# Performance work log

Measured on AMD Instinct MI355X. Metric: run time of the kernel, lower is better.

The kernel has to match this reference:

```python
import jax, jax.numpy as jnp
import numpy as np

NUM_GENES = 4384
D_MODEL = 128


def setup_inputs() -> dict:
    key = jax.random.key(0)
    ks = jax.random.split(key, 8)
    B = 8
    return {
        "mutation_input": jax.random.normal(ks[0], (B, NUM_GENES, 4), dtype=jnp.float32),
        "external_V": jax.random.normal(ks[1], (NUM_GENES, D_MODEL), dtype=jnp.float32),
        "W_in": jax.random.normal(ks[2], (4, D_MODEL), dtype=jnp.float32) * 0.5,
        "b_in": jnp.zeros((D_MODEL,), dtype=jnp.float32),
        "key_param": jax.random.normal(ks[3], (NUM_GENES, D_MODEL), dtype=jnp.float32),
        "W1": jax.random.normal(ks[4], (D_MODEL, 64), dtype=jnp.float32) * (1.0 / np.sqrt(D_MODEL)),
        "b1": jnp.zeros((64,), dtype=jnp.float32),
        "W2": jax.random.normal(ks[5], (64, 26), dtype=jnp.float32) * 0.125,
        "b2": jnp.zeros((26,), dtype=jnp.float32),
    }


def reference(mutation_input, external_V, W_in, b_in, key_param, W1, b1, W2, b2):
    # Q: [B, G, D]
    Q = jnp.einsum("bgf,fd->bgd", mutation_input, W_in) + b_in
    scale = 1.0 / jnp.sqrt(jnp.asarray(Q.shape[-1], Q.dtype))
    # scores: [B, G, G] -- full matrix as in the original module
    scores = jnp.einsum("bqd,kd->bqk", Q, key_param) * scale
    attn = jax.nn.softmax(scores, axis=-1)
    # attention output: [B, G, D]
    attn_out = jnp.einsum("bqk,kd->bqd", attn, external_V)
    mean_out = attn_out.mean(axis=1)  # [B, D]
    h = jax.nn.gelu(mean_out @ W1 + b1, approximate=False)
    out = h @ W2 + b2  # [B, 26]
    return out
```

## Files before the change

### kernel.cpp

```cpp
#include <hip/hip_runtime.h>
#include <hip/hip_bf16.h>

#define NUM_GENES 4384
#define GPAD 4608
#define DM 128
#define ROWB 256
#define LDS_STRIDE 272
#define NTILES 137
#define RB_BLOCKS 18
#define NCHUNK 6
#define TPC 23

typedef __attribute__((ext_vector_type(8))) short short8;
typedef __attribute__((ext_vector_type(16))) float floatx16;

#if defined(__has_builtin)
#  if __has_builtin(__builtin_amdgcn_exp2f)
#    define FAST_EXP2(x) __builtin_amdgcn_exp2f(x)
#  endif
#endif
#ifndef FAST_EXP2
#  define FAST_EXP2(x) exp2f(x)
#endif

static __device__ __forceinline__ short bf16bits(float x) {
    __hip_bfloat16 h = __float2bfloat16(x);
    return *(short*)&h;
}

__global__ __launch_bounds__(256)
void prep_all(const float* __restrict__ mut, const float* __restrict__ W_in,
              const float* __restrict__ b_in, const float* __restrict__ key,
              __hip_bfloat16* __restrict__ Qb, __hip_bfloat16* __restrict__ Kb,
              float* __restrict__ l, float* __restrict__ w, float* __restrict__ meanbuf) {
    int bx = blockIdx.x, t = threadIdx.x;
    if (bx < 2304) {
        int i = bx * 256 + t;
        int d0 = (i & 15) * 8;
        int g = (i >> 4) % GPAD;
        int b = i / (GPAD * 16);
        short8 o;
        if (g < NUM_GENES) {
            const float4 mv = *(const float4*)(mut + ((size_t)b * NUM_GENES + g) * 4);
            const float sc = 0.08838834764831845f * 1.4426950408889634f;
#pragma unroll
            for (int j = 0; j < 8; ++j) {
                int d = d0 + j;
                float v = b_in[d] + mv.x * W_in[d] + mv.y * W_in[128 + d]
                                  + mv.z * W_in[256 + d] + mv.w * W_in[384 + d];
                o[j] = bf16bits(v * sc);
            }
        } else {
#pragma unroll
            for (int j = 0; j < 8; ++j) o[j] = 0;
        }
        *(short8*)((short*)Qb + (size_t)i * 8) = o;
    } else if (bx < 2592) {
        int i = (bx - 2304) * 256 + t;
        int g = i >> 4;
        short8 o;
        if (g < NUM_GENES) {
            const float4 k0 = *(const float4*)(key + (size_t)i * 8);
            const float4 k1 = *(const float4*)(key + (size_t)i * 8 + 4);
            o[0] = bf16bits(k0.x); o[1] = bf16bits(k0.y);
            o[2] = bf16bits(k0.z); o[3] = bf16bits(k0.w);
            o[4] = bf16bits(k1.x); o[5] = bf16bits(k1.y);
            o[6] = bf16bits(k1.z); o[7] = bf16bits(k1.w);
        } else {
#pragma unroll
            for (int j = 0; j < 8; ++j) o[j] = 0;
        }
        *(short8*)((short*)Kb + (size_t)i * 8) = o;
    } else {
        int i = (bx - 2592) * 256 + t;
        float4 z = {0.f, 0.f, 0.f, 0.f};
        *(float4*)(l + (size_t)i * 8) = z;
        *(float4*)(l + (size_t)i * 8 + 4) = z;
        *(float4*)(w + (size_t)i * 8) = z;
        *(float4*)(w + (size_t)i * 8 + 4) = z;
        if (bx == 2592 && t < 128) {
            *(float4*)(meanbuf + t * 8) = z;
            *(float4*)(meanbuf + t * 8 + 4) = z;
        }
    }
}

template <bool PB>
__global__ __launch_bounds__(256)
void phase_kernel(const __hip_bfloat16* __restrict__ Qb,
                  const __hip_bfloat16* __restrict__ Kb,
                  const float* __restrict__ lsum,
                  float* __restrict__ out) {
    __shared__ __align__(16) char tile[2][32 * LDS_STRIDE];

    int rb    = blockIdx.x;
    int chunk = blockIdx.y;
    int b     = blockIdx.z;

    const char* resident = (const char*)(PB ? Kb : (Qb + (size_t)b * GPAD * DM));
    const char* stream   = (const char*)(PB ? (Qb + (size_t)b * GPAD * DM) : Kb);

    int t = threadIdx.x;
    int lane = t & 63, wid = t >> 6;
    int m = lane & 31, half = lane >> 5;

    short8 afrag[2][8];
#pragma unroll
    for (int g = 0; g < 2; ++g) {
        const char* arow = resident + (size_t)(rb * 256 + wid * 64 + g * 32 + m) * ROWB;
#pragma unroll
        for (int dsl = 0; dsl < 8; ++dsl)
            afrag[g][dsl] = *(const short8*)(arow + dsl * 32 + half * 16);
    }

    float lacc[2][16];
#pragma unroll
    for (int g = 0; g < 2; ++g)
#pragma unroll
        for (int r = 0; r < 16; ++r) lacc[g][r] = 0.f;

    int t0 = chunk * TPC;
    int t1 = min(NTILES, t0 + TPC);
    int sr = t >> 3, sc = t & 7;
    int soff = sr * LDS_STRIDE + sc * 32;

    {
        const char* src = stream + (size_t)(t0 * 32 + sr) * ROWB + sc * 32;
        float4 v0 = *(const float4*)src;
        float4 v1 = *(const float4*)(src + 16);
        *(float4*)(tile[0] + soff) = v0;
        *(float4*)(tile[0] + soff + 16) = v1;
    }

    int p = 0;
    for (int kt = t0; kt < t1; ++kt) {
        bool more = (kt + 1 < t1);
        float4 v0, v1;
        if (more) {
            const char* s2 = stream + (size_t)((kt + 1) * 32 + sr) * ROWB + sc * 32;
            v0 = *(const float4*)s2;
            v1 = *(const float4*)(s2 + 16);
        }
        __syncthreads();

        floatx16 acc0, acc1;
#pragma unroll
        for (int r = 0; r < 16; ++r) { acc0[r] = 0.f; acc1[r] = 0.f; }
#pragma unroll
        for (int dsl = 0; dsl < 8; ++dsl) {
            short8 bfrag = *(const short8*)(tile[p] + m * LDS_STRIDE + dsl * 32 + half * 16);
            acc0 = __builtin_amdgcn_mfma_f32_32x32x16_bf16(afrag[0][dsl], bfrag, acc0, 0, 0, 0);
            acc1 = __builtin_amdgcn_mfma_f32_32x32x16_bf16(afrag[1][dsl], bfrag, acc1, 0, 0, 0);
        }

        if (more) {
            *(float4*)(tile[p ^ 1] + soff) = v0;
            *(float4*)(tile[p ^ 1] + soff + 16) = v1;
        }

        if (PB) {
            float scl = 1.0f / lsum[b * GPAD + kt * 32 + m];
#pragma unroll
            for (int r = 0; r < 16; ++r) {
                lacc[0][r] = fmaf(FAST_EXP2(acc0[r]), scl, lacc[0][r]);
                lacc[1][r] = fmaf(FAST_EXP2(acc1[r]), scl, lacc[1][r]);
            }
        } else {
#pragma unroll
            for (int r = 0; r < 16; ++r) {
                lacc[0][r] += FAST_EXP2(acc0[r]);
                lacc[1][r] += FAST_EXP2(acc1[r]);
            }
        }
        p ^= 1;
    }

#pragma unroll
    for (int off = 1; off <= 16; off <<= 1)
#pragma unroll
        for (int g = 0; g < 2; ++g)
#pragma unroll
            for (int r = 0; r < 16; ++r)
                lacc[g][r] += __shfl_xor(lacc[g][r], off, 64);

    if (m == 0) {
#pragma unroll
        for (int g = 0; g < 2; ++g) {
            float* ob = out + b * GPAD + rb * 256 + wid * 64 + g * 32 + 4 * half;
#pragma unroll
            for (int r = 0; r < 16; ++r)
                atomicAdd(ob + (r & 3) + 8 * (r >> 2), lacc[g][r]);
        }
    }
}

__global__ __launch_bounds__(256)
void mean_k(const float* __restrict__ w, const float* __restrict__ V,
            float* __restrict__ meanbuf) {
    int rb = blockIdx.x, b = blockIdx.y;
    int t = threadIdx.x;
    int d = t & 127, half = t >> 7;
    int g0 = rb * 128 + half * 64;
    int nv = NUM_GENES - g0;
    if (nv > 64) nv = 64;
    float a = 0.f;
    if (nv > 0) {
        const float* wb = w + b * GPAD + g0;
        const float* Vp = V + (size_t)g0 * 128 + d;
        for (int k = 0; k < nv; ++k)
            a += wb[k] * Vp[(size_t)k * 128];
    }
    atomicAdd(meanbuf + b * 128 + d, a);
}

__global__ void mlp_k(const float* __restrict__ meanbuf,
                      const float* __restrict__ W1, const float* __restrict__ b1,
                      const float* __restrict__ W2, const float* __restrict__ b2,
                      float* __restrict__ out) {
    int b = blockIdx.x, t = threadIdx.x;
    __shared__ float sh[64];
    const float* mb = meanbuf + b * 128;
    float s = b1[t];
    for (int d = 0; d < 128; ++d)
        s += (mb[d] * (1.0f / 4384.0f)) * W1[d * 64 + t];
    sh[t] = 0.5f * s * (1.0f + erff(s * 0.70710678118654752f));
    __syncthreads();
    if (t < 26) {
        float o = b2[t];
        for (int j = 0; j < 64; ++j) o += sh[j] * W2[j * 26 + t];
        out[b * 26 + t] = o;
    }
}

extern "C" void kernel_launch(void* const* d_in, const int* in_sizes, int n_in,
                              void* d_out, int out_size, void* d_ws, size_t ws_size,
                              hipStream_t stream) {
    const float* mut  = (const float*)d_in[0];
    const float* V    = (const float*)d_in[1];
    const float* W_in = (const float*)d_in[2];
    const float* b_in = (const float*)d_in[3];
    const float* key  = (const float*)d_in[4];
    const float* W1   = (const float*)d_in[5];
    const float* b1   = (const float*)d_in[6];
    const float* W2   = (const float*)d_in[7];
    const float* b2   = (const float*)d_in[8];
    float* out = (float*)d_out;

    char* ws = (char*)d_ws;
    __hip_bfloat16* Qb = (__hip_bfloat16*)(ws);
    __hip_bfloat16* Kb = (__hip_bfloat16*)(ws + 9437184);
    float* lbuf        = (float*)(ws + 10616832);
    float* wbuf        = (float*)(ws + 10764288);
    float* meanbuf     = (float*)(ws + 10911744);

    prep_all<<<2610, 256, 0, stream>>>(mut, W_in, b_in, key, Qb, Kb, lbuf, wbuf, meanbuf);

    dim3 grid(RB_BLOCKS, NCHUNK, 8);
    phase_kernel<false><<<grid, 256, 0, stream>>>(Qb, Kb, lbuf, lbuf);
    phase_kernel<true><<<grid, 256, 0, stream>>>(Qb, Kb, lbuf, wbuf);

    mean_k<<<dim3(35, 8), 256, 0, stream>>>(wbuf, V, meanbuf);
    mlp_k<<<8, 64, 0, stream>>>(meanbuf, W1, b1, W2, b2, out);
}
```

Before: 212.0 us.

## Fuse weighted-V reduction into second attention pass, drop mean kernel

The second phase kernel now writes its per-key column weights into shared memory and immediately multiplies them against V, atomically accumulating into the mean buffer. This removes the separate mean_k launch, the w buffer and its zeroing. The cost is that every chunk block (6 per row block) re-reads its 256 rows of V, and the atomic traffic on meanbuf grows. Two smaller tweaks ride along: the MFMA loop is peeled so the first step starts from a zero accumulator, and the reciprocal uses rcp.

```diff
diff --git a/kernel.cpp b/kernel.cpp
--- a/kernel.cpp
+++ b/kernel.cpp
@@ -32,7 +32,7 @@
 void prep_all(const float* __restrict__ mut, const float* __restrict__ W_in,
               const float* __restrict__ b_in, const float* __restrict__ key,
               __hip_bfloat16* __restrict__ Qb, __hip_bfloat16* __restrict__ Kb,
-              float* __restrict__ l, float* __restrict__ w, float* __restrict__ meanbuf) {
+              float* __restrict__ l, float* __restrict__ meanbuf) {
     int bx = blockIdx.x, t = threadIdx.x;
     if (bx < 2304) {
         int i = bx * 256 + t;
@@ -76,8 +76,6 @@
         float4 z = {0.f, 0.f, 0.f, 0.f};
         *(float4*)(l + (size_t)i * 8) = z;
         *(float4*)(l + (size_t)i * 8 + 4) = z;
-        *(float4*)(w + (size_t)i * 8) = z;
-        *(float4*)(w + (size_t)i * 8 + 4) = z;
         if (bx == 2592 && t < 128) {
             *(float4*)(meanbuf + t * 8) = z;
             *(float4*)(meanbuf + t * 8 + 4) = z;
@@ -90,8 +88,10 @@
 void phase_kernel(const __hip_bfloat16* __restrict__ Qb,
                   const __hip_bfloat16* __restrict__ Kb,
                   const float* __restrict__ lsum,
+                  const float* __restrict__ V,
                   float* __restrict__ out) {
     __shared__ __align__(16) char tile[2][32 * LDS_STRIDE];
+    __shared__ float sw[256];
 
     int rb    = blockIdx.x;
     int chunk = blockIdx.y;
@@ -112,6 +112,10 @@
         for (int dsl = 0; dsl < 8; ++dsl)
             afrag[g][dsl] = *(const short8*)(arow + dsl * 32 + half * 16);
     }
+
+    floatx16 z;
+#pragma unroll
+    for (int r = 0; r < 16; ++r) z[r] = 0.f;
 
     float lacc[2][16];
 #pragma unroll
@@ -143,23 +147,25 @@
         }
         __syncthreads();
 
-        floatx16 acc0, acc1;
-#pragma unroll
-        for (int r = 0; r < 16; ++r) { acc0[r] = 0.f; acc1[r] = 0.f; }
-#pragma unroll
-        for (int dsl = 0; dsl < 8; ++dsl) {
-            short8 bfrag = *(const short8*)(tile[p] + m * LDS_STRIDE + dsl * 32 + half * 16);
+        const char* tp = tile[p];
+        short8 bfrag = *(const short8*)(tp + m * LDS_STRIDE + half * 16);
+        floatx16 acc0 = __builtin_amdgcn_mfma_f32_32x32x16_bf16(afrag[0][0], bfrag, z, 0, 0, 0);
+        floatx16 acc1 = __builtin_amdgcn_mfma_f32_32x32x16_bf16(afrag[1][0], bfrag, z, 0, 0, 0);
+#pragma unroll
+        for (int dsl = 1; dsl < 8; ++dsl) {
+            bfrag = *(const short8*)(tp + m * LDS_STRIDE + dsl * 32 + half * 16);
             acc0 = __builtin_amdgcn_mfma_f32_32x32x16_bf16(afrag[0][dsl], bfrag, acc0, 0, 0, 0);
             acc1 = __builtin_amdgcn_mfma_f32_32x32x16_bf16(afrag[1][dsl], bfrag, acc1, 0, 0, 0);
         }
 
         if (more) {
-            *(float4*)(tile[p ^ 1] + soff) = v0;
-            *(float4*)(tile[p ^ 1] + soff + 16) = v1;
+            char* tn = tile[p ^ 1];
+            *(float4*)(tn + soff) = v0;
+            *(float4*)(tn + soff + 16) = v1;
         }
 
         if (PB) {
-            float scl = 1.0f / lsum[b * GPAD + kt * 32 + m];
+            float scl = __builtin_amdgcn_rcpf(lsum[b * GPAD + kt * 32 + m]);
 #pragma unroll
             for (int r = 0; r < 16; ++r) {
                 lacc[0][r] = fmaf(FAST_EXP2(acc0[r]), scl, lacc[0][r]);
@@ -183,34 +189,47 @@
             for (int r = 0; r < 16; ++r)
                 lacc[g][r] += __shfl_xor(lacc[g][r], off, 64);
 
-    if (m == 0) {
-#pragma unroll
-        for (int g = 0; g < 2; ++g) {
-            float* ob = out + b * GPAD + rb * 256 + wid * 64 + g * 32 + 4 * half;
-#pragma unroll
-            for (int r = 0; r < 16; ++r)
-                atomicAdd(ob + (r & 3) + 8 * (r >> 2), lacc[g][r]);
-        }
-    }
-}
-
-__global__ __launch_bounds__(256)
-void mean_k(const float* __restrict__ w, const float* __restrict__ V,
-            float* __restrict__ meanbuf) {
-    int rb = blockIdx.x, b = blockIdx.y;
-    int t = threadIdx.x;
-    int d = t & 127, half = t >> 7;
-    int g0 = rb * 128 + half * 64;
-    int nv = NUM_GENES - g0;
-    if (nv > 64) nv = 64;
-    float a = 0.f;
-    if (nv > 0) {
-        const float* wb = w + b * GPAD + g0;
-        const float* Vp = V + (size_t)g0 * 128 + d;
-        for (int k = 0; k < nv; ++k)
-            a += wb[k] * Vp[(size_t)k * 128];
-    }
-    atomicAdd(meanbuf + b * 128 + d, a);
+    if (!PB) {
+        if (m == 0) {
+#pragma unroll
+            for (int g = 0; g < 2; ++g) {
+                float* ob = out + b * GPAD + rb * 256 + wid * 64 + g * 32 + 4 * half;
+#pragma unroll
+                for (int r = 0; r < 16; ++r)
+                    atomicAdd(ob + (r & 3) + 8 * (r >> 2), lacc[g][r]);
+            }
+        }
+    } else {
+        __syncthreads();
+        if (m == 0) {
+#pragma unroll
+            for (int g = 0; g < 2; ++g) {
+                int base = wid * 64 + g * 32 + 4 * half;
+#pragma unroll
+                for (int r = 0; r < 16; ++r) {
+                    int rl = base + (r & 3) + 8 * (r >> 2);
+                    sw[rl] = (rb * 256 + rl < NUM_GENES) ? lacc[g][r] : 0.f;
+                }
+            }
+        }
+        __syncthreads();
+        int d = t & 127, hf = t >> 7;
+        int gbase = rb * 256 + hf * 128;
+        int cnt = NUM_GENES - gbase;
+        if (cnt > 128) cnt = 128;
+        if (cnt > 0) {
+            const float* swp = sw + hf * 128;
+            const float* Vp = V + (size_t)gbase * 128 + d;
+            float a0 = 0.f, a1 = 0.f;
+            int k = 0;
+            for (; k + 1 < cnt; k += 2) {
+                a0 += swp[k] * Vp[(size_t)k * 128];
+                a1 += swp[k + 1] * Vp[(size_t)(k + 1) * 128];
+            }
+            if (k < cnt) a0 += swp[k] * Vp[(size_t)k * 128];
+            atomicAdd(out + b * 128 + d, a0 + a1);
+        }
+    }
 }
 
 __global__ void mlp_k(const float* __restrict__ meanbuf,
@@ -250,15 +269,13 @@
     __hip_bfloat16* Qb = (__hip_bfloat16*)(ws);
     __hip_bfloat16* Kb = (__hip_bfloat16*)(ws + 9437184);
     float* lbuf        = (float*)(ws + 10616832);
-    float* wbuf        = (float*)(ws + 10764288);
-    float* meanbuf     = (float*)(ws + 10911744);
-
-    prep_all<<<2610, 256, 0, stream>>>(mut, W_in, b_in, key, Qb, Kb, lbuf, wbuf, meanbuf);
+    float* meanbuf     = (float*)(ws + 10764288);
+
+    prep_all<<<2610, 256, 0, stream>>>(mut, W_in, b_in, key, Qb, Kb, lbuf, meanbuf);
 
     dim3 grid(RB_BLOCKS, NCHUNK, 8);
-    phase_kernel<false><<<grid, 256, 0, stream>>>(Qb, Kb, lbuf, lbuf);
-    phase_kernel<true><<<grid, 256, 0, stream>>>(Qb, Kb, lbuf, wbuf);
-
-    mean_k<<<dim3(35, 8), 256, 0, stream>>>(wbuf, V, meanbuf);
+    phase_kernel<false><<<grid, 256, 0, stream>>>(Qb, Kb, lbuf, V, lbuf);
+    phase_kernel<true><<<grid, 256, 0, stream>>>(Qb, Kb, lbuf, V, meanbuf);
+
     mlp_k<<<8, 64, 0, stream>>>(meanbuf, W1, b1, W2, b2, out);
 }
```

Result: slower. 220.4 us (+4.0%).
